# Kernel optimization log

Measured on AMD Instinct MI355X. Metric: run time of the kernel, lower is better.

The kernel has to match this reference:

```python
import jax, jax.numpy as jnp
import numpy as np


def l2norm(x):
    return x * jax.lax.rsqrt(jnp.sum(x * x, axis=-1, keepdims=True) + 1e-12)


def vq_cosine(z, codebook, commit_w):
    # cosine-sim VQ: normalize inputs + codebook, nearest neighbor by cosine sim
    xn = l2norm(z)            # [N, D]
    en = l2norm(codebook)     # [K, D]
    sim = xn @ en.T           # [N, K]
    dist = 2.0 - 2.0 * sim    # squared euclidean between unit vectors
    idx = jnp.argmin(dist, axis=-1)           # [N]
    q = en[idx]                               # [N, D] quantized (normalized) codes
    commit = commit_w * jnp.mean((jax.lax.stop_gradient(q) - xn) ** 2)
    q_st = xn + jax.lax.stop_gradient(q - xn)  # straight-through
    return q_st, idx, commit, dist


def setup_inputs() -> dict:
    key = jax.random.key(0)
    ks = jax.random.split(key, 10)
    N, Din, H, K = 32768, 1024, 512, 1024
    s = lambda i, shp, fan: jax.random.normal(ks[i], shp, jnp.float32) * (1.0 / np.sqrt(fan))
    return {
        "h0": jax.random.normal(ks[0], (N, Din), jnp.float32),
        "W1": s(1, (Din, H), Din), "b1": jnp.zeros((H,), jnp.float32),
        "W2": s(2, (H, H), H),     "b2": jnp.zeros((H,), jnp.float32),
        "Wm": s(3, (H, H), H),     "bm": jnp.zeros((H,), jnp.float32),
        "Wt": s(4, (H, H), H),     "bt": jnp.zeros((H,), jnp.float32),
        "Wp": s(5, (H, H), H),     "bp": jnp.zeros((H,), jnp.float32),
        "cb_m": jax.random.normal(ks[6], (K, H), jnp.float32),
        "cb_t": jax.random.normal(ks[7], (K, H), jnp.float32),
        "cb_p": jax.random.normal(ks[8], (K, H), jnp.float32),
        "Wk": s(9, (H, 1), H),     "bk": jnp.zeros((1,), jnp.float32),
    }


def reference(h0, W1, b1, W2, b2, Wm, bm, Wt, bt, Wp, bp, cb_m, cb_t, cb_p, Wk, bk):
    COMMIT = 0.25
    TOP_M = 32
    # encoder: Linear-ReLU-Linear-ReLU
    H = jax.nn.relu(jax.nn.relu(h0 @ W1 + b1) @ W2 + b2)
    z_m = H @ Wm + bm
    z_t = H @ Wt + bt
    z_p = H @ Wp + bp
    q_m, k_m, cm, dist_m = vq_cosine(z_m, cb_m, COMMIT)
    q_t, k_t, ct, dist_t = vq_cosine(z_t, cb_t, COMMIT)
    q_p, k_p, cp, dist_p = vq_cosine(z_p, cb_p, COMMIT)
    codes = jnp.stack([k_m, k_t, k_p], axis=-1)           # [N, 3]
    alpha = jax.nn.sigmoid((H @ Wk + bk)[:, 0])           # [N]
    M = min(TOP_M, alpha.shape[0])
    key_idx = jax.lax.top_k(alpha, M)[1]                  # [M]
    token_emb = jnp.concatenate([q_m, q_t, q_p], axis=-1) # [N, 3*hid]
    L_vq = cm + ct + cp
    return (H, codes, key_idx, token_emb, L_vq)
```

## Files before the change

### kernel.cpp

```cpp
#include <hip/hip_runtime.h>


#define BM 128
#define MAXF 4096
#define MAXF1 12288
#define TAU_DIST 2e-5f
#define TAU_APPROX 1.25e-4f

#define CODES_OFF   16777216ULL
#define KEYIDX_OFF  16875520ULL
#define TOKEMB_OFF  16875552ULL
#define LVQ_OFF     67207200ULL

typedef __attribute__((ext_vector_type(8))) short short8;
typedef __attribute__((ext_vector_type(4))) float f32x4;

#define MFMA_BF16(a, b, c) __builtin_amdgcn_mfma_f32_16x16x32_bf16(a, b, c, 0, 0, 0)

__device__ __forceinline__ unsigned flip_bits(float x) {
  unsigned b = __float_as_uint(x);
  return b ^ ((unsigned)((int)b >> 31) | 0x80000000u);
}
__device__ __forceinline__ float unflip_bits(unsigned ob) {
  unsigned b = (ob & 0x80000000u) ? (ob ^ 0x80000000u) : ~ob;
  return __uint_as_float(b);
}
__device__ __forceinline__ float qdist(float dot, float rnv) {
  float sim = __fmul_rn(dot, rnv);
  return __fadd_rn(2.0f, -__fmul_rn(2.0f, sim));
}
__device__ __forceinline__ float dist_of_key(unsigned long long q) {
  return unflip_bits(~(unsigned)(q >> 32));
}
__device__ __forceinline__ void split2(float x, unsigned& h, unsigned& l) {
  unsigned b = __float_as_uint(x);
  unsigned hb = (b + 0x7FFFu + ((b >> 16) & 1u)) & 0xFFFF0000u;
  h = hb >> 16;
  float r = x - __uint_as_float(hb);
  unsigned cbits = __float_as_uint(r);
  l = (cbits + 0x7FFFu + ((cbits >> 16) & 1u)) >> 16;
}

__global__ __launch_bounds__(256)
void wsplit_g(const float* __restrict__ W,
              unsigned short* __restrict__ wh, unsigned short* __restrict__ wl,
              int K)
{
  int t = blockIdx.x * 256 + threadIdx.x;
  int kg8 = K >> 3;
  int n = t / kg8, kg = (t % kg8) * 8;
  unsigned h[8], l[8];
#pragma unroll
  for (int i = 0; i < 8; i++) {
    float v = W[(size_t)(kg + i) * 512 + n];
    split2(v, h[i], l[i]);
  }
  uint4 hp, lp;
  hp.x = h[0] | (h[1] << 16); hp.y = h[2] | (h[3] << 16);
  hp.z = h[4] | (h[5] << 16); hp.w = h[6] | (h[7] << 16);
  lp.x = l[0] | (l[1] << 16); lp.y = l[2] | (l[3] << 16);
  lp.z = l[4] | (l[5] << 16); lp.w = l[6] | (l[7] << 16);
  size_t g = (size_t)n * K + kg;
  *(uint4*)(wh + g) = hp;
  *(uint4*)(wl + g) = lp;
}

template<int RELU, int OUTPLANES>
__global__ __launch_bounds__(512, 2)
void mfma_gemm(const float* __restrict__ A, int lda, int K,
               const unsigned short* __restrict__ wh,
               const unsigned short* __restrict__ wl,
               const float* __restrict__ bias,
               float* __restrict__ Cf, int ldc,
               unsigned short* __restrict__ zh, unsigned short* __restrict__ zl,
               int ldz, int colOff)
{
  __shared__ __align__(16) unsigned char smem[102400];
  unsigned short* Ah = (unsigned short*)smem;
  unsigned short* Al = Ah + 5120;
  unsigned short* Bh = Al + 5120;
  unsigned short* Bl = Bh + 20480;

  const int tid = threadIdx.x;
  const int w = tid >> 6, wr = w >> 2, wc = w & 3;
  const int l = tid & 63, l15 = l & 15, lg = l >> 4;
  const long m0 = (long)blockIdx.x * BM;

  f32x4 acc[4][8];
#pragma unroll
  for (int fi = 0; fi < 4; fi++)
#pragma unroll
    for (int fj = 0; fj < 8; fj++)
#pragma unroll
      for (int r = 0; r < 4; r++) acc[fi][fj][r] = 0.f;

  for (int k0 = 0; k0 < K; k0 += 32) {
#pragma unroll
    for (int i = 0; i < 2; i++) {
      int f4 = tid + i * 512;
      int row = f4 >> 3, kc = (f4 & 7) * 4;
      float4 v = *(const float4*)(A + (m0 + row) * lda + k0 + kc);
      unsigned hx, lx, hy, ly, hz, lz, hw, lw;
      split2(v.x, hx, lx); split2(v.y, hy, ly);
      split2(v.z, hz, lz); split2(v.w, hw, lw);
      uint2 hp, lp;
      hp.x = hx | (hy << 16); hp.y = hz | (hw << 16);
      lp.x = lx | (ly << 16); lp.y = lz | (lw << 16);
      *(uint2*)&Ah[row * 40 + kc] = hp;
      *(uint2*)&Al[row * 40 + kc] = lp;
    }
#pragma unroll
    for (int j = 0; j < 4; j++) {
      int q = tid + j * 512;
      int n = q >> 2, kg = (q & 3) * 8;
      size_t g = (size_t)n * K + k0 + kg;
      *(uint4*)&Bh[n * 40 + kg] = *(const uint4*)(wh + g);
      *(uint4*)&Bl[n * 40 + kg] = *(const uint4*)(wl + g);
    }
    __syncthreads();

    short8 bh[8], bl[8];
#pragma unroll
    for (int fj = 0; fj < 8; fj++) {
      int boff = (wc * 128 + fj * 16 + l15) * 40 + lg * 8;
      bh[fj] = *(const short8*)&Bh[boff];
      bl[fj] = *(const short8*)&Bl[boff];
    }
#pragma unroll
    for (int fi = 0; fi < 4; fi++) {
      int aoff = (wr * 64 + fi * 16 + l15) * 40 + lg * 8;
      short8 ah = *(const short8*)&Ah[aoff];
      short8 al = *(const short8*)&Al[aoff];
#pragma unroll
      for (int fj = 0; fj < 8; fj++) {
        acc[fi][fj] = MFMA_BF16(ah, bh[fj], acc[fi][fj]);
        acc[fi][fj] = MFMA_BF16(al, bh[fj], acc[fi][fj]);
        acc[fi][fj] = MFMA_BF16(ah, bl[fj], acc[fi][fj]);
      }
    }
    __syncthreads();
  }

  float bcv[8];
#pragma unroll
  for (int fj = 0; fj < 8; fj++) bcv[fj] = bias[wc * 128 + fj * 16 + l15];

  if (OUTPLANES == 0) {
#pragma unroll
    for (int fi = 0; fi < 4; fi++)
#pragma unroll
      for (int fj = 0; fj < 8; fj++) {
        int col = wc * 128 + fj * 16 + l15;
#pragma unroll
        for (int r = 0; r < 4; r++) {
          long row = m0 + wr * 64 + fi * 16 + lg * 4 + r;
          float v = acc[fi][fj][r] + bcv[fj];
          if (RELU) v = fmaxf(v, 0.f);
          Cf[row * (long)ldc + col] = v;
        }
      }
  } else {
    unsigned short* ep = (unsigned short*)smem;
#pragma unroll
    for (int half = 0; half < 2; half++) {
#pragma unroll
      for (int pl = 0; pl < 2; pl++) {
        if (wr == half) {
#pragma unroll
          for (int fi = 0; fi < 4; fi++)
#pragma unroll
            for (int fj = 0; fj < 8; fj++) {
              int col = wc * 128 + fj * 16 + l15;
#pragma unroll
              for (int r = 0; r < 4; r++) {
                int row = fi * 16 + lg * 4 + r;
                float v = acc[fi][fj][r] + bcv[fj];
                unsigned h, lo;
                split2(v, h, lo);
                ep[row * 512 + col] = (unsigned short)(pl ? lo : h);
              }
            }
        }
        __syncthreads();
        unsigned short* dst = pl ? zl : zh;
        for (int u = tid; u < 4096; u += 512) {
          int row = u >> 6, c8 = (u & 63) * 8;
          size_t g = (size_t)(m0 + half * 64 + row) * ldz + colOff + c8;
          *(uint4*)(dst + g) = *(const uint4*)(ep + row * 512 + c8);
        }
        __syncthreads();
      }
    }
  }
}

__global__ __launch_bounds__(256)
void sim_argmax(const unsigned short* __restrict__ zh,
                const unsigned short* __restrict__ zl,
                const float* __restrict__ en,
                const unsigned short* __restrict__ en_hi,
                const unsigned short* __restrict__ en_lo,
                const float* __restrict__ rn,
                float* __restrict__ out,
                float* __restrict__ lvq,
                int* __restrict__ fc1,
                int* __restrict__ flags1)
{
  __shared__ unsigned short Ah[128 * 40];
  __shared__ unsigned short Al[128 * 40];
  __shared__ unsigned short Bh[128 * 40];
  __shared__ unsigned short Bl[128 * 40];
  __shared__ unsigned long long redk[128][2];
  __shared__ float redd[128][2];
  __shared__ int bidx[128];
  __shared__ float dsum[128];

  const int tid = threadIdx.x;
  const int w = tid >> 6, wr = w >> 1, wc = w & 1;
  const int l = tid & 63, l15 = l & 15, lg = l >> 4;
  const int c = blockIdx.y;
  const long m0 = (long)blockIdx.x * BM;
  const float* Ben = en + (size_t)c * 524288;
  const size_t cb_base = (size_t)c * 524288;

  float rrn[16];
#pragma unroll
  for (int fi = 0; fi < 4; fi++)
#pragma unroll
    for (int r = 0; r < 4; r++)
      rrn[fi * 4 + r] = rn[(long)c * 32768 + m0 + wr * 64 + fi * 16 + lg * 4 + r];

  unsigned long long best = 0ULL;
  float bestd2 = 1e30f;

  for (int ct = 0; ct < 8; ct++) {
    const int n0 = ct * 128;
    f32x4 acc[4][4];
#pragma unroll
    for (int fi = 0; fi < 4; fi++)
#pragma unroll
      for (int fj = 0; fj < 4; fj++)
#pragma unroll
        for (int r = 0; r < 4; r++) acc[fi][fj][r] = 0.f;

    for (int k0 = 0; k0 < 512; k0 += 32) {
#pragma unroll
      for (int i = 0; i < 2; i++) {
        int q = tid + i * 256;
        int row = q >> 2, kc = (q & 3) * 8;
        size_t g = (size_t)(m0 + row) * 1536 + (size_t)c * 512 + k0 + kc;
        *(uint4*)&Ah[row * 40 + kc] = *(const uint4*)(zh + g);
        *(uint4*)&Al[row * 40 + kc] = *(const uint4*)(zl + g);
      }
#pragma unroll
      for (int i = 0; i < 2; i++) {
        int q = tid + i * 256;
        int code = q >> 2, kc = (q & 3) * 8;
        size_t g = cb_base + (size_t)(n0 + code) * 512 + (k0 + kc);
        *(uint4*)&Bh[code * 40 + kc] = *(const uint4*)(en_hi + g);
        *(uint4*)&Bl[code * 40 + kc] = *(const uint4*)(en_lo + g);
      }
      __syncthreads();

      short8 bh[4], bl[4];
#pragma unroll
      for (int f = 0; f < 4; f++) {
        int boff = (wc * 64 + f * 16 + l15) * 40 + lg * 8;
        bh[f] = *(const short8*)&Bh[boff];
        bl[f] = *(const short8*)&Bl[boff];
      }
#pragma unroll
      for (int fi = 0; fi < 4; fi++) {
        int aoff = (wr * 64 + fi * 16 + l15) * 40 + lg * 8;
        short8 ah = *(const short8*)&Ah[aoff];
        short8 al = *(const short8*)&Al[aoff];
#pragma unroll
        for (int fj = 0; fj < 4; fj++) {
          acc[fi][fj] = MFMA_BF16(ah, bh[fj], acc[fi][fj]);
          acc[fi][fj] = MFMA_BF16(al, bh[fj], acc[fi][fj]);
          acc[fi][fj] = MFMA_BF16(ah, bl[fj], acc[fi][fj]);
        }
      }
      __syncthreads();
    }

#pragma unroll
    for (int fi = 0; fi < 4; fi++) {
      unsigned long long kk[4]; float dd[4];
#pragma unroll
      for (int r = 0; r < 4; r++) {
        float d1 = 1e30f, d2v = 1e30f; int bj = 0;
#pragma unroll
        for (int fj = 0; fj < 4; fj++) {
          float d = qdist(acc[fi][fj][r], rrn[fi * 4 + r]);
          if (d < d1) { d2v = d1; d1 = d; bj = fj; }
          else if (d < d2v) d2v = d;
        }
        int code = n0 + wc * 64 + bj * 16 + l15;
        kk[r] = ((unsigned long long)(~flip_bits(d1)) << 32) | (unsigned)(~code);
        dd[r] = d2v;
      }
#pragma unroll
      for (int m = 1; m < 16; m <<= 1) {
#pragma unroll
        for (int r = 0; r < 4; r++) {
          unsigned long long ok = __shfl_xor(kk[r], m, 64);
          float od = __shfl_xor(dd[r], m, 64);
          if (ok > kk[r]) { dd[r] = fminf(od, dist_of_key(kk[r])); kk[r] = ok; }
          else dd[r] = fminf(dd[r], dist_of_key(ok));
        }
      }
      if (l15 == 0) {
#pragma unroll
        for (int r = 0; r < 4; r++) {
          int row = wr * 64 + fi * 16 + lg * 4 + r;
          redk[row][wc] = kk[r];
          redd[row][wc] = dd[r];
        }
      }
    }
    __syncthreads();
    if (tid < 128) {
      unsigned long long kA = redk[tid][0]; float dA = redd[tid][0];
      unsigned long long kB = redk[tid][1]; float dB = redd[tid][1];
      unsigned long long km; float m2;
      if (kB > kA) { km = kB; m2 = fminf(dB, dist_of_key(kA)); }
      else         { km = kA; m2 = fminf(dA, dist_of_key(kB)); }
      if (km > best) {
        float oldd = (best == 0ULL) ? 1e30f : dist_of_key(best);
        bestd2 = fminf(oldd, m2);
        best = km;
      } else {
        bestd2 = fminf(bestd2, dist_of_key(km));
      }
    }
    __syncthreads();
  }

  if (tid < 128) {
    const long n = m0 + tid;
    const unsigned code = ~(unsigned)best;
    const float d1 = dist_of_key(best);
    out[CODES_OFF + (unsigned long long)n * 3 + c] = (float)code;
    bidx[tid] = (int)code;
    dsum[tid] = d1;
    if (bestd2 - d1 < TAU_APPROX) {
      int slot = atomicAdd(fc1, 1);
      if (slot < MAXF1) { flags1[2 * slot] = (int)n; flags1[2 * slot + 1] = c; }
    }
  }
  __syncthreads();
  if (tid < 64) dsum[tid] += dsum[tid + 64];
  __syncthreads();
  if (tid < 64) {
    float s = dsum[tid];
#pragma unroll
    for (int off = 32; off; off >>= 1) s += __shfl_xor(s, off);
    if (tid == 0) atomicAdd(lvq, s * (0.25f / (32768.f * 512.f)));
  }
  for (int t = tid; t < 128 * 128; t += 256) {
    int r = t >> 7, d4 = (t & 127) * 4;
    float4 v = *(const float4*)(Ben + (long)bidx[r] * 512 + d4);
    *(float4*)(out + TOKEMB_OFF + (unsigned long long)(m0 + r) * 1536 + c * 512 + d4) = v;
  }
}

__global__ __launch_bounds__(256)
void refine_fp32(const float* __restrict__ H,
                 const float* __restrict__ Wm, const float* __restrict__ bm,
                 const float* __restrict__ Wt, const float* __restrict__ bt,
                 const float* __restrict__ Wp, const float* __restrict__ bp,
                 const float* __restrict__ en,
                 const int* __restrict__ fc1, const int* __restrict__ flags1,
                 int* __restrict__ fc2, int* __restrict__ flags2,
                 float* __restrict__ out)
{
  int nf = *fc1; if (nf > MAXF1) nf = MAXF1;
  const int b = blockIdx.x;
  if (b >= nf) return;
  const int n = flags1[2 * b];
  const int c = flags1[2 * b + 1];
  const int t = threadIdx.x;

  __shared__ float sH[512];
  __shared__ float zs[512];
  __shared__ float sred[256];
  __shared__ unsigned long long wk[4];
  __shared__ float wd2[4];
  __shared__ int fcode;
  __shared__ float srn;

  const float* Wc = (c == 0) ? Wm : (c == 1) ? Wt : Wp;
  const float* bc = (c == 0) ? bm : (c == 1) ? bt : bp;

  sH[t]       = H[(size_t)n * 512 + t];
  sH[t + 256] = H[(size_t)n * 512 + 256 + t];
  __syncthreads();

  {
    float a0 = 0.f, a1 = 0.f;
    for (int i = 0; i < 512; i++) {
      float h = sH[i];
      a0 = fmaf(h, Wc[(size_t)i * 512 + t], a0);
      a1 = fmaf(h, Wc[(size_t)i * 512 + t + 256], a1);
    }
    float z0 = a0 + bc[t];
    float z1 = a1 + bc[t + 256];
    zs[t] = z0; zs[t + 256] = z1;
    sred[t] = z0 * z0 + z1 * z1;
  }
  __syncthreads();
  for (int s = 128; s > 0; s >>= 1) {
    if (t < s) sred[t] += sred[t + s];
    __syncthreads();
  }
  if (t == 0) srn = 1.f / sqrtf(sred[0] + 1e-12f);
  __syncthreads();
  const float rnv = srn;

  const int wv = t >> 6, lane = t & 63;
  float zlv[8];
#pragma unroll
  for (int m = 0; m < 8; m++) zlv[m] = zs[lane * 8 + m];

  const float* cbase = en + (size_t)c * 524288;
  unsigned long long k1 = 0ULL; float d2 = 1e30f;
  for (int j = 0; j < 256; j++) {
    int k = (j << 2) | wv;
    const float* cr = cbase + (size_t)k * 512 + lane * 8;
    float4 c0 = *(const float4*)cr, c1 = *(const float4*)(cr + 4);
    float dt = zlv[0] * c0.x + zlv[1] * c0.y + zlv[2] * c0.z + zlv[3] * c0.w
             + zlv[4] * c1.x + zlv[5] * c1.y + zlv[6] * c1.z + zlv[7] * c1.w;
#pragma unroll
    for (int off = 32; off; off >>= 1) dt += __shfl_xor(dt, off);
    float d = qdist(dt, rnv);
    unsigned long long key =
        ((unsigned long long)(~flip_bits(d)) << 32) | (unsigned)(~k);
    if (key > k1) { d2 = fminf(d2, (k1 == 0ULL) ? 1e30f : dist_of_key(k1)); k1 = key; }
    else d2 = fminf(d2, d);
  }
  if (lane == 0) { wk[wv] = k1; wd2[wv] = d2; }
  __syncthreads();
  if (t == 0) {
    unsigned long long kb = wk[0]; float s2 = wd2[0];
#pragma unroll
    for (int w = 1; w < 4; w++) {
      unsigned long long q = wk[w]; float qd2 = wd2[w];
      if (q > kb) { s2 = fminf(qd2, dist_of_key(kb)); kb = q; }
      else s2 = fminf(s2, dist_of_key(q));
    }
    int code = (int)(~(unsigned)kb);
    float d1 = dist_of_key(kb);
    out[CODES_OFF + (unsigned long long)n * 3 + c] = (float)code;
    fcode = code;
    if (s2 - d1 < TAU_DIST) {
      int slot = atomicAdd(fc2, 1);
      if (slot < MAXF) { flags2[2 * slot] = n; flags2[2 * slot + 1] = c; }
    }
  }
  __syncthreads();
  const int fk = fcode;
  if (t < 128) {
    const float* er = en + ((size_t)c * 1024 + fk) * 512;
    float4 v = ((const float4*)er)[t];
    *(float4*)(out + TOKEMB_OFF + (unsigned long long)n * 1536 + c * 512 + t * 4) = v;
  }
}

__global__ __launch_bounds__(256)
void rescue_fp64(const float* __restrict__ h0,
                 const float* __restrict__ W1, const float* __restrict__ b1,
                 const float* __restrict__ W2, const float* __restrict__ b2,
                 const float* __restrict__ Wm, const float* __restrict__ bm,
                 const float* __restrict__ Wt, const float* __restrict__ bt,
                 const float* __restrict__ Wp, const float* __restrict__ bp,
                 const float* __restrict__ cbm, const float* __restrict__ cbt,
                 const float* __restrict__ cbp,
                 const float* __restrict__ en,
                 const int* __restrict__ flag_cnt, const int* __restrict__ flags,
                 float* __restrict__ out)
{
  int nf = *flag_cnt; if (nf > MAXF) nf = MAXF;
  const int b = blockIdx.x;
  if (b >= nf) return;
  const int n = flags[2 * b];
  const int c = flags[2 * b + 1];
  const int t = threadIdx.x;

  __shared__ double s1[512];
  __shared__ double s2[512];
  __shared__ double sred[256];
  __shared__ float sd4[4];
  __shared__ int sk4[4];
  __shared__ double shz;

  const float* Wc = (c == 0) ? Wm : (c == 1) ? Wt : Wp;
  const float* bc = (c == 0) ? bm : (c == 1) ? bt : bp;
  const float* cb = (c == 0) ? cbm : (c == 1) ? cbt : cbp;
  const float* h0r = h0 + (size_t)n * 1024;

  {
    double a0 = 0.0, a1 = 0.0;
    for (int i = 0; i < 1024; i++) {
      double h = (double)h0r[i];
      a0 = fma(h, (double)W1[(size_t)i * 512 + t], a0);
      a1 = fma(h, (double)W1[(size_t)i * 512 + t + 256], a1);
    }
    s1[t]       = fmax(a0 + (double)b1[t], 0.0);
    s1[t + 256] = fmax(a1 + (double)b1[t + 256], 0.0);
  }
  __syncthreads();
  {
    double a0 = 0.0, a1 = 0.0;
    for (int i = 0; i < 512; i++) {
      double h = s1[i];
      a0 = fma(h, (double)W2[(size_t)i * 512 + t], a0);
      a1 = fma(h, (double)W2[(size_t)i * 512 + t + 256], a1);
    }
    s2[t]       = fmax(a0 + (double)b2[t], 0.0);
    s2[t + 256] = fmax(a1 + (double)b2[t + 256], 0.0);
  }
  __syncthreads();
  {
    double a0 = 0.0, a1 = 0.0;
    for (int i = 0; i < 512; i++) {
      double h = s2[i];
      a0 = fma(h, (double)Wc[(size_t)i * 512 + t], a0);
      a1 = fma(h, (double)Wc[(size_t)i * 512 + t + 256], a1);
    }
    __syncthreads();
    s1[t]       = a0 + (double)bc[t];
    s1[t + 256] = a1 + (double)bc[t + 256];
  }
  __syncthreads();
  sred[t] = s1[t] * s1[t] + s1[t + 256] * s1[t + 256];
  __syncthreads();
  for (int s = 128; s > 0; s >>= 1) {
    if (t < s) sred[t] += sred[t + s];
    __syncthreads();
  }
  if (t == 0) shz = 1.0 / sqrt(sred[0] + 1e-12);
  __syncthreads();
  const double rz = shz;

  const int wv = t >> 6, lane = t & 63;
  double zl[8];
#pragma unroll
  for (int m = 0; m < 8; m++) zl[m] = s1[lane * 8 + m];
  float bd = 1e30f; int bkk = 1 << 30;
  for (int j = 0; j < 256; j++) {
    int k = (j << 2) | wv;
    const float* cr = cb + (size_t)k * 512 + lane * 8;
    float4 c0 = *(const float4*)cr, c1 = *(const float4*)(cr + 4);
    double x0 = c0.x, x1 = c0.y, x2 = c0.z, x3 = c0.w;
    double x4 = c1.x, x5 = c1.y, x6 = c1.z, x7 = c1.w;
    double dt = zl[0]*x0 + zl[1]*x1 + zl[2]*x2 + zl[3]*x3
              + zl[4]*x4 + zl[5]*x5 + zl[6]*x6 + zl[7]*x7;
    double nc = x0*x0 + x1*x1 + x2*x2 + x3*x3 + x4*x4 + x5*x5 + x6*x6 + x7*x7;
#pragma unroll
    for (int off = 32; off; off >>= 1) {
      dt += __shfl_xor(dt, off);
      nc += __shfl_xor(nc, off);
    }
    double sim64 = dt * rz * (1.0 / sqrt(nc + 1e-12));
    float s32 = (float)sim64;
    float d32 = __fadd_rn(2.0f, -__fmul_rn(2.0f, s32));
    if (d32 < bd) { bd = d32; bkk = k; }
  }
  if (lane == 0) { sd4[wv] = bd; sk4[wv] = bkk; }
  __syncthreads();
  if (t == 0) {
    float d = sd4[0]; int k = sk4[0];
#pragma unroll
    for (int w = 1; w < 4; w++)
      if (sd4[w] < d || (sd4[w] == d && sk4[w] < k)) { d = sd4[w]; k = sk4[w]; }
    sk4[0] = k;
    out[CODES_OFF + (unsigned long long)n * 3 + c] = (float)k;
  }
  __syncthreads();
  const int fk = sk4[0];
  if (t < 128) {
    const float* er = en + ((size_t)c * 1024 + fk) * 512;
    float4 v = ((const float4*)er)[t];
    *(float4*)(out + TOKEMB_OFF + (unsigned long long)n * 1536 + c * 512 + t * 4) = v;
  }
}

__global__ __launch_bounds__(256)
void row_rnorm(const unsigned short* __restrict__ zh,
               const unsigned short* __restrict__ zl,
               float* __restrict__ rn)
{
  const int lane = threadIdx.x & 63;
  const long r = (long)blockIdx.x * 4 + (threadIdx.x >> 6);
  const int cc = (int)(r >> 15), n = (int)(r & 32767);
  const size_t base = (size_t)n * 1536 + (size_t)cc * 512 + lane * 8;
  uint4 h = *(const uint4*)(zh + base);
  uint4 lo = *(const uint4*)(zl + base);
  float s = 0.f;
  const unsigned hw[4] = {h.x, h.y, h.z, h.w};
  const unsigned lw[4] = {lo.x, lo.y, lo.z, lo.w};
#pragma unroll
  for (int i = 0; i < 4; i++) {
    float ze = __uint_as_float(hw[i] << 16) + __uint_as_float(lw[i] << 16);
    float zo = __uint_as_float(hw[i] & 0xFFFF0000u) + __uint_as_float(lw[i] & 0xFFFF0000u);
    s = fmaf(ze, ze, s);
    s = fmaf(zo, zo, s);
  }
#pragma unroll
  for (int off = 32; off; off >>= 1) s += __shfl_xor(s, off);
  if (lane == 0) rn[r] = 1.f / sqrtf(s + 1e-12f);
}

__global__ __launch_bounds__(256)
void cb_norm(const float* __restrict__ cbm, const float* __restrict__ cbt,
             const float* __restrict__ cbp, float* __restrict__ en,
             unsigned short* __restrict__ en_hi, unsigned short* __restrict__ en_lo)
{
  const int lane = threadIdx.x & 63;
  const long r = (long)blockIdx.x * 4 + (threadIdx.x >> 6);
  const int cc = (int)(r >> 10), k = (int)(r & 1023);
  const float* cb = (cc == 0) ? cbm : (cc == 1) ? cbt : cbp;
  const float* p = cb + (long)k * 512 + lane * 8;
  float4 v0 = *(const float4*)p, v1 = *(const float4*)(p + 4);
  float s = v0.x * v0.x + v0.y * v0.y + v0.z * v0.z + v0.w * v0.w
          + v1.x * v1.x + v1.y * v1.y + v1.z * v1.z + v1.w * v1.w;
#pragma unroll
  for (int off = 32; off; off >>= 1) s += __shfl_xor(s, off);
  float sc = 1.f / sqrtf(s + 1e-12f);
  v0.x *= sc; v0.y *= sc; v0.z *= sc; v0.w *= sc;
  v1.x *= sc; v1.y *= sc; v1.z *= sc; v1.w *= sc;
  const size_t g = (size_t)cc * 524288 + (size_t)k * 512 + lane * 8;
  float* q = en + g;
  *(float4*)q = v0; *(float4*)(q + 4) = v1;
  unsigned h[8], lo[8];
  split2(v0.x, h[0], lo[0]); split2(v0.y, h[1], lo[1]);
  split2(v0.z, h[2], lo[2]); split2(v0.w, h[3], lo[3]);
  split2(v1.x, h[4], lo[4]); split2(v1.y, h[5], lo[5]);
  split2(v1.z, h[6], lo[6]); split2(v1.w, h[7], lo[7]);
  uint4 hp, lp;
  hp.x = h[0] | (h[1] << 16);  hp.y = h[2] | (h[3] << 16);
  hp.z = h[4] | (h[5] << 16);  hp.w = h[6] | (h[7] << 16);
  lp.x = lo[0] | (lo[1] << 16); lp.y = lo[2] | (lo[3] << 16);
  lp.z = lo[4] | (lo[5] << 16); lp.w = lo[6] | (lo[7] << 16);
  *(uint4*)(en_hi + g) = hp;
  *(uint4*)(en_lo + g) = lp;
}

__global__ __launch_bounds__(256)
void logits_alpha(const float* __restrict__ H, const float* __restrict__ Wk,
                  const float* __restrict__ bk, float* __restrict__ alpha)
{
  const int lane = threadIdx.x & 63;
  const long n = (long)blockIdx.x * 4 + (threadIdx.x >> 6);
  const float* p = H + n * 512 + lane * 8;
  const float* w = Wk + lane * 8;
  float4 a0 = *(const float4*)p, a1 = *(const float4*)(p + 4);
  float4 w0 = *(const float4*)w, w1 = *(const float4*)(w + 4);
  float s = a0.x * w0.x + a0.y * w0.y + a0.z * w0.z + a0.w * w0.w
          + a1.x * w1.x + a1.y * w1.y + a1.z * w1.z + a1.w * w1.w;
#pragma unroll
  for (int off = 32; off; off >>= 1) s += __shfl_xor(s, off);
  if (lane == 0) alpha[n] = 1.f / (1.f + expf(-(s + bk[0])));
}

__global__ __launch_bounds__(1024)
void topk32(const float* __restrict__ alpha, float* __restrict__ out)
{
  __shared__ unsigned long long sk[1024];
  const int tid = threadIdx.x;
  unsigned long long prev = ~0ULL;
  for (int it = 0; it < 32; it++) {
    unsigned long long best = 0;
#pragma unroll 4
    for (int i = tid; i < 32768; i += 1024) {
      unsigned long long key =
          ((unsigned long long)flip_bits(alpha[i]) << 32) | (unsigned)(~i);
      if (key < prev && key > best) best = key;
    }
    sk[tid] = best;
    __syncthreads();
    for (int s = 512; s > 0; s >>= 1) {
      if (tid < s) { unsigned long long q = sk[tid + s]; if (q > sk[tid]) sk[tid] = q; }
      __syncthreads();
    }
    unsigned long long sel = sk[0];
    __syncthreads();
    if (tid == 0) out[it] = (float)(~(unsigned)sel);
    prev = sel;
  }
}

extern "C" void kernel_launch(void* const* d_in, const int* in_sizes, int n_in,
                              void* d_out, int out_size, void* d_ws, size_t ws_size,
                              hipStream_t stream)
{
  (void)in_sizes; (void)n_in; (void)out_size; (void)ws_size;
  const float* h0  = (const float*)d_in[0];
  const float* W1  = (const float*)d_in[1];
  const float* b1  = (const float*)d_in[2];
  const float* W2  = (const float*)d_in[3];
  const float* b2  = (const float*)d_in[4];
  const float* Wm  = (const float*)d_in[5];
  const float* bm  = (const float*)d_in[6];
  const float* Wt  = (const float*)d_in[7];
  const float* bt  = (const float*)d_in[8];
  const float* Wp  = (const float*)d_in[9];
  const float* bp  = (const float*)d_in[10];
  const float* cbm = (const float*)d_in[11];
  const float* cbt = (const float*)d_in[12];
  const float* cbp = (const float*)d_in[13];
  const float* Wk  = (const float*)d_in[14];
  const float* bk  = (const float*)d_in[15];
  float* out = (float*)d_out;
  float* ws  = (float*)d_ws;

  unsigned short* zh = (unsigned short*)ws;
  unsigned short* zl = (unsigned short*)ws + 50331648ULL;
  float* h1 = ws;
  unsigned short* W1h = (unsigned short*)ws + 33554432ULL;
  unsigned short* W1l = W1h + 524288ULL;
  unsigned short* W2h = W1l + 524288ULL;
  unsigned short* W2l = W2h + 262144ULL;
  float* en = ws + 50331648ULL;
  float* rn = ws + 51904512ULL;
  float* al = ws + 52002816ULL;
  int* fc1    = (int*)(ws + 52035584ULL);
  int* flags1 = (int*)(ws + 52035585ULL);
  int* fc2    = (int*)(ws + 52060161ULL);
  int* flags2 = (int*)(ws + 52060162ULL);
  unsigned short* en_hi = (unsigned short*)(ws + 52068356ULL);
  unsigned short* en_lo = (unsigned short*)(ws + 52854788ULL);
  unsigned short* Wh = (unsigned short*)(ws + 53641220ULL);
  unsigned short* Wl = (unsigned short*)(ws + 54034436ULL);
  float* H  = out;
  float* lvq = out + LVQ_OFF;

  hipMemsetAsync(lvq, 0, sizeof(float), stream);
  hipMemsetAsync(fc1, 0, sizeof(int), stream);
  hipMemsetAsync(fc2, 0, sizeof(int), stream);

  wsplit_g<<<256, 256, 0, stream>>>(W1, W1h, W1l, 1024);
  wsplit_g<<<128, 256, 0, stream>>>(W2, W2h, W2l, 512);
  wsplit_g<<<128, 256, 0, stream>>>(Wm, Wh + 0 * 262144, Wl + 0 * 262144, 512);
  wsplit_g<<<128, 256, 0, stream>>>(Wt, Wh + 1 * 262144, Wl + 1 * 262144, 512);
  wsplit_g<<<128, 256, 0, stream>>>(Wp, Wh + 2 * 262144, Wl + 2 * 262144, 512);

  mfma_gemm<1, 0><<<256, 512, 0, stream>>>(h0, 1024, 1024, W1h, W1l, b1,
                                           h1, 512, nullptr, nullptr, 0, 0);
  mfma_gemm<1, 0><<<256, 512, 0, stream>>>(h1, 512, 512, W2h, W2l, b2,
                                           H, 512, nullptr, nullptr, 0, 0);

  mfma_gemm<0, 1><<<256, 512, 0, stream>>>(H, 512, 512, Wh + 0 * 262144,
                                           Wl + 0 * 262144, bm, nullptr, 0,
                                           zh, zl, 1536, 0);
  mfma_gemm<0, 1><<<256, 512, 0, stream>>>(H, 512, 512, Wh + 1 * 262144,
                                           Wl + 1 * 262144, bt, nullptr, 0,
                                           zh, zl, 1536, 512);
  mfma_gemm<0, 1><<<256, 512, 0, stream>>>(H, 512, 512, Wh + 2 * 262144,
                                           Wl + 2 * 262144, bp, nullptr, 0,
                                           zh, zl, 1536, 1024);

  row_rnorm<<<24576, 256, 0, stream>>>(zh, zl, rn);
  cb_norm<<<768, 256, 0, stream>>>(cbm, cbt, cbp, en, en_hi, en_lo);
  sim_argmax<<<dim3(256, 3), 256, 0, stream>>>(zh, zl, en, en_hi, en_lo, rn, out, lvq,
                                               fc1, flags1);
  refine_fp32<<<MAXF1, 256, 0, stream>>>(H, Wm, bm, Wt, bt, Wp, bp, en,
                                         fc1, flags1, fc2, flags2, out);
  rescue_fp64<<<MAXF, 256, 0, stream>>>(h0, W1, b1, W2, b2, Wm, bm, Wt, bt, Wp, bp,
                                        cbm, cbt, cbp, en, fc2, flags2, out);
  logits_alpha<<<8192, 256, 0, stream>>>(H, Wk, bk, al);
  topk32<<<1, 1024, 0, stream>>>(al, out + KEYIDX_OFF);
}
```

Measured before the change: 2.304 ms.

## Retile encoder GEMMs to 128x128 blocks, merge weight-split launches, register-cache topk keys

The encoder and projection GEMMs move from 128x512 output tiles with 512 threads to 128x128 tiles with 256 threads over a 2D grid. This quadruples the block count from 256 to 1024 and cuts LDS use per block, which should improve occupancy and CU fill. Five weight-split launches become one kernel, and the two counter memsets are merged by placing the counters next to each other. topk32 now keeps its 32 keys per thread in registers instead of re-reading alpha on every iteration. The cost is that each A tile is re-read and re-split four times across column blocks, and register pressure rises in topk.

Result: faster. 2.065 ms (-10.4%).

```diff
diff --git a/kernel.cpp b/kernel.cpp
--- a/kernel.cpp
+++ b/kernel.cpp
@@ -42,13 +42,27 @@
 }
 
 __global__ __launch_bounds__(256)
-void wsplit_g(const float* __restrict__ W,
-              unsigned short* __restrict__ wh, unsigned short* __restrict__ wl,
-              int K)
+void wsplit_all(const float* __restrict__ W1, const float* __restrict__ W2,
+                const float* __restrict__ Wm, const float* __restrict__ Wt,
+                const float* __restrict__ Wp,
+                unsigned short* __restrict__ w1h, unsigned short* __restrict__ w1l,
+                unsigned short* __restrict__ w2h, unsigned short* __restrict__ w2l,
+                unsigned short* __restrict__ wh,  unsigned short* __restrict__ wl)
 {
   int t = blockIdx.x * 256 + threadIdx.x;
-  int kg8 = K >> 3;
-  int n = t / kg8, kg = (t % kg8) * 8;
+  const float* W; unsigned short *dh, *dl; int n, kg, K;
+  if (t < 65536) {
+    W = W1; dh = w1h; dl = w1l; K = 1024;
+    n = t >> 7; kg = (t & 127) * 8;
+  } else {
+    int idx = t - 65536;
+    int w = idx >> 15, rem = idx & 32767;
+    n = rem >> 6; kg = (rem & 63) * 8; K = 512;
+    if (w == 0)      { W = W2; dh = w2h;          dl = w2l; }
+    else if (w == 1) { W = Wm; dh = wh;           dl = wl; }
+    else if (w == 2) { W = Wt; dh = wh + 262144;  dl = wl + 262144; }
+    else             { W = Wp; dh = wh + 524288;  dl = wl + 524288; }
+  }
   unsigned h[8], l[8];
 #pragma unroll
   for (int i = 0; i < 8; i++) {
@@ -61,43 +75,44 @@
   lp.x = l[0] | (l[1] << 16); lp.y = l[2] | (l[3] << 16);
   lp.z = l[4] | (l[5] << 16); lp.w = l[6] | (l[7] << 16);
   size_t g = (size_t)n * K + kg;
-  *(uint4*)(wh + g) = hp;
-  *(uint4*)(wl + g) = lp;
+  *(uint4*)(dh + g) = hp;
+  *(uint4*)(dl + g) = lp;
 }
 
 template<int RELU, int OUTPLANES>
-__global__ __launch_bounds__(512, 2)
-void mfma_gemm(const float* __restrict__ A, int lda, int K,
-               const unsigned short* __restrict__ wh,
-               const unsigned short* __restrict__ wl,
-               const float* __restrict__ bias,
-               float* __restrict__ Cf, int ldc,
-               unsigned short* __restrict__ zh, unsigned short* __restrict__ zl,
-               int ldz, int colOff)
-{
-  __shared__ __align__(16) unsigned char smem[102400];
+__global__ __launch_bounds__(256)
+void mfma_gemm128(const float* __restrict__ A, int lda, int K,
+                  const unsigned short* __restrict__ wh,
+                  const unsigned short* __restrict__ wl,
+                  const float* __restrict__ bias,
+                  float* __restrict__ Cf, int ldc,
+                  unsigned short* __restrict__ zh, unsigned short* __restrict__ zl,
+                  int ldz, int colOff)
+{
+  __shared__ __align__(16) unsigned char smem[40960];
   unsigned short* Ah = (unsigned short*)smem;
   unsigned short* Al = Ah + 5120;
   unsigned short* Bh = Al + 5120;
-  unsigned short* Bl = Bh + 20480;
+  unsigned short* Bl = Bh + 5120;
 
   const int tid = threadIdx.x;
-  const int w = tid >> 6, wr = w >> 2, wc = w & 3;
+  const int w = tid >> 6, wr = w >> 1, wc = w & 1;
   const int l = tid & 63, l15 = l & 15, lg = l >> 4;
   const long m0 = (long)blockIdx.x * BM;
-
-  f32x4 acc[4][8];
+  const int n0 = blockIdx.y * 128;
+
+  f32x4 acc[4][4];
 #pragma unroll
   for (int fi = 0; fi < 4; fi++)
 #pragma unroll
-    for (int fj = 0; fj < 8; fj++)
+    for (int fj = 0; fj < 4; fj++)
 #pragma unroll
       for (int r = 0; r < 4; r++) acc[fi][fj][r] = 0.f;
 
   for (int k0 = 0; k0 < K; k0 += 32) {
 #pragma unroll
-    for (int i = 0; i < 2; i++) {
-      int f4 = tid + i * 512;
+    for (int i = 0; i < 4; i++) {
+      int f4 = tid + i * 256;
       int row = f4 >> 3, kc = (f4 & 7) * 4;
       float4 v = *(const float4*)(A + (m0 + row) * lda + k0 + kc);
       unsigned hx, lx, hy, ly, hz, lz, hw, lw;
@@ -110,21 +125,21 @@
       *(uint2*)&Al[row * 40 + kc] = lp;
     }
 #pragma unroll
-    for (int j = 0; j < 4; j++) {
-      int q = tid + j * 512;
-      int n = q >> 2, kg = (q & 3) * 8;
-      size_t g = (size_t)n * K + k0 + kg;
-      *(uint4*)&Bh[n * 40 + kg] = *(const uint4*)(wh + g);
-      *(uint4*)&Bl[n * 40 + kg] = *(const uint4*)(wl + g);
-    }
-    __syncthreads();
-
-    short8 bh[8], bl[8];
-#pragma unroll
-    for (int fj = 0; fj < 8; fj++) {
-      int boff = (wc * 128 + fj * 16 + l15) * 40 + lg * 8;
-      bh[fj] = *(const short8*)&Bh[boff];
-      bl[fj] = *(const short8*)&Bl[boff];
+    for (int i = 0; i < 2; i++) {
+      int q = tid + i * 256;
+      int code = q >> 2, kc = (q & 3) * 8;
+      size_t g = (size_t)(n0 + code) * K + k0 + kc;
+      *(uint4*)&Bh[code * 40 + kc] = *(const uint4*)(wh + g);
+      *(uint4*)&Bl[code * 40 + kc] = *(const uint4*)(wl + g);
+    }
+    __syncthreads();
+
+    short8 bh[4], bl[4];
+#pragma unroll
+    for (int f = 0; f < 4; f++) {
+      int boff = (wc * 64 + f * 16 + l15) * 40 + lg * 8;
+      bh[f] = *(const short8*)&Bh[boff];
+      bl[f] = *(const short8*)&Bl[boff];
     }
 #pragma unroll
     for (int fi = 0; fi < 4; fi++) {
@@ -132,7 +147,7 @@
       short8 ah = *(const short8*)&Ah[aoff];
       short8 al = *(const short8*)&Al[aoff];
 #pragma unroll
-      for (int fj = 0; fj < 8; fj++) {
+      for (int fj = 0; fj < 4; fj++) {
         acc[fi][fj] = MFMA_BF16(ah, bh[fj], acc[fi][fj]);
         acc[fi][fj] = MFMA_BF16(al, bh[fj], acc[fi][fj]);
         acc[fi][fj] = MFMA_BF16(ah, bl[fj], acc[fi][fj]);
@@ -141,16 +156,16 @@
     __syncthreads();
   }
 
-  float bcv[8];
-#pragma unroll
-  for (int fj = 0; fj < 8; fj++) bcv[fj] = bias[wc * 128 + fj * 16 + l15];
+  float bcv[4];
+#pragma unroll
+  for (int fj = 0; fj < 4; fj++) bcv[fj] = bias[n0 + wc * 64 + fj * 16 + l15];
 
   if (OUTPLANES == 0) {
 #pragma unroll
     for (int fi = 0; fi < 4; fi++)
 #pragma unroll
-      for (int fj = 0; fj < 8; fj++) {
-        int col = wc * 128 + fj * 16 + l15;
+      for (int fj = 0; fj < 4; fj++) {
+        int col = n0 + wc * 64 + fj * 16 + l15;
 #pragma unroll
         for (int r = 0; r < 4; r++) {
           long row = m0 + wr * 64 + fi * 16 + lg * 4 + r;
@@ -162,34 +177,29 @@
   } else {
     unsigned short* ep = (unsigned short*)smem;
 #pragma unroll
-    for (int half = 0; half < 2; half++) {
-#pragma unroll
-      for (int pl = 0; pl < 2; pl++) {
-        if (wr == half) {
-#pragma unroll
-          for (int fi = 0; fi < 4; fi++)
-#pragma unroll
-            for (int fj = 0; fj < 8; fj++) {
-              int col = wc * 128 + fj * 16 + l15;
-#pragma unroll
-              for (int r = 0; r < 4; r++) {
-                int row = fi * 16 + lg * 4 + r;
-                float v = acc[fi][fj][r] + bcv[fj];
-                unsigned h, lo;
-                split2(v, h, lo);
-                ep[row * 512 + col] = (unsigned short)(pl ? lo : h);
-              }
-            }
+    for (int pl = 0; pl < 2; pl++) {
+#pragma unroll
+      for (int fi = 0; fi < 4; fi++)
+#pragma unroll
+        for (int fj = 0; fj < 4; fj++) {
+          int lcol = wc * 64 + fj * 16 + l15;
+#pragma unroll
+          for (int r = 0; r < 4; r++) {
+            int lrow = wr * 64 + fi * 16 + lg * 4 + r;
+            float v = acc[fi][fj][r] + bcv[fj];
+            unsigned h, lo;
+            split2(v, h, lo);
+            ep[lrow * 128 + lcol] = (unsigned short)(pl ? lo : h);
+          }
         }
-        __syncthreads();
-        unsigned short* dst = pl ? zl : zh;
-        for (int u = tid; u < 4096; u += 512) {
-          int row = u >> 6, c8 = (u & 63) * 8;
-          size_t g = (size_t)(m0 + half * 64 + row) * ldz + colOff + c8;
-          *(uint4*)(dst + g) = *(const uint4*)(ep + row * 512 + c8);
-        }
-        __syncthreads();
-      }
+      __syncthreads();
+      unsigned short* dst = pl ? zl : zh;
+      for (int u = tid; u < 2048; u += 256) {
+        int row = u >> 4, c8 = (u & 15) * 8;
+        size_t g = (size_t)(m0 + row) * ldz + colOff + n0 + c8;
+        *(uint4*)(dst + g) = *(const uint4*)(ep + row * 128 + c8);
+      }
+      __syncthreads();
     }
   }
 }
@@ -669,15 +679,18 @@
 {
   __shared__ unsigned long long sk[1024];
   const int tid = threadIdx.x;
+  unsigned long long key[32];
+#pragma unroll
+  for (int j = 0; j < 32; j++) {
+    int i = tid + j * 1024;
+    key[j] = ((unsigned long long)flip_bits(alpha[i]) << 32) | (unsigned)(~i);
+  }
   unsigned long long prev = ~0ULL;
   for (int it = 0; it < 32; it++) {
     unsigned long long best = 0;
-#pragma unroll 4
-    for (int i = tid; i < 32768; i += 1024) {
-      unsigned long long key =
-          ((unsigned long long)flip_bits(alpha[i]) << 32) | (unsigned)(~i);
-      if (key < prev && key > best) best = key;
-    }
+#pragma unroll
+    for (int j = 0; j < 32; j++)
+      if (key[j] < prev && key[j] > best) best = key[j];
     sk[tid] = best;
     __syncthreads();
     for (int s = 512; s > 0; s >>= 1) {
@@ -726,9 +739,9 @@
   float* rn = ws + 51904512ULL;
   float* al = ws + 52002816ULL;
   int* fc1    = (int*)(ws + 52035584ULL);
-  int* flags1 = (int*)(ws + 52035585ULL);
-  int* fc2    = (int*)(ws + 52060161ULL);
-  int* flags2 = (int*)(ws + 52060162ULL);
+  int* fc2    = fc1 + 1;
+  int* flags1 = fc1 + 2;
+  int* flags2 = flags1 + 2 * MAXF1;
   unsigned short* en_hi = (unsigned short*)(ws + 52068356ULL);
   unsigned short* en_lo = (unsigned short*)(ws + 52854788ULL);
   unsigned short* Wh = (unsigned short*)(ws + 53641220ULL);
@@ -737,29 +750,25 @@
   float* lvq = out + LVQ_OFF;
 
   hipMemsetAsync(lvq, 0, sizeof(float), stream);
-  hipMemsetAsync(fc1, 0, sizeof(int), stream);
-  hipMemsetAsync(fc2, 0, sizeof(int), stream);
-
-  wsplit_g<<<256, 256, 0, stream>>>(W1, W1h, W1l, 1024);
-  wsplit_g<<<128, 256, 0, stream>>>(W2, W2h, W2l, 512);
-  wsplit_g<<<128, 256, 0, stream>>>(Wm, Wh + 0 * 262144, Wl + 0 * 262144, 512);
-  wsplit_g<<<128, 256, 0, stream>>>(Wt, Wh + 1 * 262144, Wl + 1 * 262144, 512);
-  wsplit_g<<<128, 256, 0, stream>>>(Wp, Wh + 2 * 262144, Wl + 2 * 262144, 512);
-
-  mfma_gemm<1, 0><<<256, 512, 0, stream>>>(h0, 1024, 1024, W1h, W1l, b1,
-                                           h1, 512, nullptr, nullptr, 0, 0);
-  mfma_gemm<1, 0><<<256, 512, 0, stream>>>(h1, 512, 512, W2h, W2l, b2,
-                                           H, 512, nullptr, nullptr, 0, 0);
-
-  mfma_gemm<0, 1><<<256, 512, 0, stream>>>(H, 512, 512, Wh + 0 * 262144,
-                                           Wl + 0 * 262144, bm, nullptr, 0,
-                                           zh, zl, 1536, 0);
-  mfma_gemm<0, 1><<<256, 512, 0, stream>>>(H, 512, 512, Wh + 1 * 262144,
-                                           Wl + 1 * 262144, bt, nullptr, 0,
-                                           zh, zl, 1536, 512);
-  mfma_gemm<0, 1><<<256, 512, 0, stream>>>(H, 512, 512, Wh + 2 * 262144,
-                                           Wl + 2 * 262144, bp, nullptr, 0,
-                                           zh, zl, 1536, 1024);
+  hipMemsetAsync(fc1, 0, 2 * sizeof(int), stream);
+
+  wsplit_all<<<768, 256, 0, stream>>>(W1, W2, Wm, Wt, Wp,
+                                      W1h, W1l, W2h, W2l, Wh, Wl);
+
+  mfma_gemm128<1, 0><<<dim3(256, 4), 256, 0, stream>>>(
+      h0, 1024, 1024, W1h, W1l, b1, h1, 512, nullptr, nullptr, 0, 0);
+  mfma_gemm128<1, 0><<<dim3(256, 4), 256, 0, stream>>>(
+      h1, 512, 512, W2h, W2l, b2, H, 512, nullptr, nullptr, 0, 0);
+
+  mfma_gemm128<0, 1><<<dim3(256, 4), 256, 0, stream>>>(
+      H, 512, 512, Wh + 0 * 262144, Wl + 0 * 262144, bm, nullptr, 0,
+      zh, zl, 1536, 0);
+  mfma_gemm128<0, 1><<<dim3(256, 4), 256, 0, stream>>>(
+      H, 512, 512, Wh + 1 * 262144, Wl + 1 * 262144, bt, nullptr, 0,
+      zh, zl, 1536, 512);
+  mfma_gemm128<0, 1><<<dim3(256, 4), 256, 0, stream>>>(
+      H, 512, 512, Wh + 2 * 262144, Wl + 2 * 262144, bp, nullptr, 0,
+      zh, zl, 1536, 1024);
 
   row_rnorm<<<24576, 256, 0, stream>>>(zh, zl, rn);
   cb_norm<<<768, 256, 0, stream>>>(cbm, cbt, cbp, en, en_hi, en_lo);
```
